# Optimization experiments

Measured on AMD Instinct MI355X. Metric: run time of the kernel, lower is better.

Reference implementation:

```python
import jax, jax.numpy as jnp
import numpy as np

N, E, HDIM, EDIM, MSG_H, UPD_H = 50000, 640000, 128, 32, 128, 128
LN_EPS = 1e-5


def setup_inputs() -> dict:
    key = jax.random.key(0)
    ks = jax.random.split(key, 12)
    def lin(k, fan_in, fan_out):
        return jax.random.normal(k, (fan_in, fan_out), dtype=jnp.float32) / np.sqrt(fan_in)
    h = jax.random.normal(ks[0], (N, HDIM), dtype=jnp.float32)
    edge_index = jax.random.randint(ks[1], (2, E), 0, N, dtype=jnp.int32)
    edge_attr = jax.random.normal(ks[2], (E, EDIM), dtype=jnp.float32)
    return {
        "h": h,
        "edge_index": edge_index,
        "edge_attr": edge_attr,
        # edge MLP: Linear(2*hdim+edim -> msg_hidden), ReLU, Linear(msg_hidden -> hdim)
        "ew1": lin(ks[3], 2 * HDIM + EDIM, MSG_H),
        "eb1": jnp.zeros((MSG_H,), jnp.float32),
        "ew2": lin(ks[4], MSG_H, HDIM),
        "eb2": jnp.zeros((HDIM,), jnp.float32),
        # node MLP: Linear(2*hdim -> upd_hidden), ReLU, Linear(upd_hidden -> hdim)
        "nw1": lin(ks[5], 2 * HDIM, UPD_H),
        "nb1": jnp.zeros((UPD_H,), jnp.float32),
        "nw2": lin(ks[6], UPD_H, HDIM),
        "nb2": jnp.zeros((HDIM,), jnp.float32),
        # LayerNorm(hdim)
        "gamma": jnp.ones((HDIM,), jnp.float32),
        "beta": jnp.zeros((HDIM,), jnp.float32),
    }


def reference(h, edge_index, edge_attr, ew1, eb1, ew2, eb2, nw1, nb1, nw2, nb2, gamma, beta):
    src, dst = edge_index[0], edge_index[1]
    # gather + concat -> edge MLP  (eval mode: dropout inactive, edge_dropout off)
    m_in = jnp.concatenate([h[src], h[dst], edge_attr], axis=1)       # [E, 2H+EDIM]
    m = jax.nn.relu(m_in @ ew1 + eb1) @ ew2 + eb2                     # [E, H]
    # scatter-add messages into destination nodes
    agg = jax.ops.segment_sum(m, dst, num_segments=h.shape[0])        # [N, H]
    # node update MLP
    u_in = jnp.concatenate([h, agg], axis=1)                          # [N, 2H]
    h_upd = jax.nn.relu(u_in @ nw1 + nb1) @ nw2 + nb2                 # [N, H]
    # residual + LayerNorm
    x = h + h_upd
    mu = jnp.mean(x, axis=-1, keepdims=True)
    var = jnp.mean(jnp.square(x - mu), axis=-1, keepdims=True)
    return (x - mu) * jax.lax.rsqrt(var + LN_EPS) * gamma + beta
```

## Files before the change

kernel.cpp:

```cpp
#include <hip/hip_runtime.h>
#include <cstdint>

#define HD 128
#define ED 32
#define BME 32
#define BMN 128
#define PAD_N 264
#define PAD_T 136
#define EGRID 512

typedef _Float16 f16;
typedef __attribute__((ext_vector_type(2))) _Float16 f16x2;
typedef __attribute__((ext_vector_type(4))) _Float16 f16x4;
typedef __attribute__((ext_vector_type(8))) _Float16 f16x8;
typedef __attribute__((ext_vector_type(4))) float    f32x4;
typedef __attribute__((ext_vector_type(4))) unsigned int u32x4;

__device__ __forceinline__ f32x4 mfma16(f16x8 a, f16x8 b, f32x4 c) {
    return __builtin_amdgcn_mfma_f32_16x16x32_f16(a, b, c, 0, 0, 0);
}
__device__ __forceinline__ f16x8 cvt8(const float* p) {
    const float4 a0 = *(const float4*)p;
    const float4 a1 = *(const float4*)(p + 4);
    f16x8 v;
    v[0] = (f16)a0.x; v[1] = (f16)a0.y; v[2] = (f16)a0.z; v[3] = (f16)a0.w;
    v[4] = (f16)a1.x; v[5] = (f16)a1.y; v[6] = (f16)a1.z; v[7] = (f16)a1.w;
    return v;
}
__device__ __forceinline__ void barrier_lds() {
    asm volatile("s_waitcnt lgkmcnt(0)" ::: "memory");
    __builtin_amdgcn_s_barrier();
    __builtin_amdgcn_sched_barrier(0);
}

__global__ __launch_bounds__(256) void zero_f32(float4* p, long n4) {
    long i = (long)blockIdx.x * blockDim.x + threadIdx.x;
    const long stride = (long)gridDim.x * blockDim.x;
    const float4 z = make_float4(0.f, 0.f, 0.f, 0.f);
    for (; i < n4; i += stride) p[i] = z;
}
__global__ __launch_bounds__(256) void zero_i32(int* p, int n) {
    int i = blockIdx.x * blockDim.x + threadIdx.x;
    if (i < n) p[i] = 0;
}
__global__ __launch_bounds__(256)
void cvt_f16_kernel(const float* __restrict__ x, f16* __restrict__ y, long n8) {
    long i = blockIdx.x * 256 + threadIdx.x;
    const long stride = (long)gridDim.x * 256;
    for (; i < n8; i += stride) *(f16x8*)(y + i * 8) = cvt8(x + i * 8);
}
__global__ __launch_bounds__(256)
void pack_all_kernel(const float* __restrict__ ew1, const float* __restrict__ ew2,
                     const float* __restrict__ nw1, const float* __restrict__ nw2,
                     f16* __restrict__ w1p, f16* __restrict__ w2p,
                     f16* __restrict__ n1p, f16* __restrict__ n2p)
{
    const int b = blockIdx.x;
    const float* w; f16* wp; int base;
    if (b < 18)      { w = ew1; wp = w1p; base = b; }
    else if (b < 26) { w = ew2; wp = w2p; base = b - 18; }
    else if (b < 42) { w = nw1; wp = n1p; base = b - 26; }
    else             { w = nw2; wp = n2p; base = b - 42; }
    const int idx = base * 256 + threadIdx.x;
    const int l  = idx & 63;
    const int fr = idx >> 6;
    const int wi = fr & 7, kt = fr >> 3;
    const int lii = l & 15, qq = l >> 4;
    const float* p = w + (size_t)(32 * kt + 8 * qq) * HD + 16 * wi + lii;
    f16x8 v;
#pragma unroll
    for (int e2 = 0; e2 < 8; ++e2) v[e2] = (f16)p[(size_t)e2 * HD];
    *(f16x8*)(wp + (size_t)idx * 8) = v;
}

__global__ __launch_bounds__(256)
void hist_kernel(const int* __restrict__ eidx, int* __restrict__ rank,
                 int* __restrict__ cnt, int E) {
    int e = blockIdx.x * 256 + threadIdx.x;
    if (e < E) rank[e] = atomicAdd(&cnt[eidx[E + e]], 1);
}
__global__ __launch_bounds__(1024)
void scan_kernel(const int* __restrict__ cnt, int* __restrict__ rs, int N) {
    __shared__ int wsum[16];
    __shared__ int s_carry;
    const int t = threadIdx.x, lane = t & 63, wid = t >> 6;
    if (t == 0) s_carry = 0;
    __syncthreads();
    for (int base = 0; base < N; base += 1024) {
        const int i = base + t;
        const int v = (i < N) ? cnt[i] : 0;
        int incl = v;
#pragma unroll
        for (int off = 1; off < 64; off <<= 1) {
            int u = __shfl_up(incl, off, 64);
            if (lane >= off) incl += u;
        }
        if (lane == 63) wsum[wid] = incl;
        __syncthreads();
        if (t == 0) {
            int s = 0;
#pragma unroll
            for (int w = 0; w < 16; ++w) { int x = wsum[w]; wsum[w] = s; s += x; }
        }
        __syncthreads();
        const int carry = s_carry;
        if (i < N) rs[i] = carry + wsum[wid] + incl - v;
        __syncthreads();
        if (t == 1023) s_carry = carry + wsum[15] + incl;
        __syncthreads();
    }
    if (threadIdx.x == 0) rs[N] = s_carry;
}
__global__ __launch_bounds__(256)
void pos_kernel(const int* __restrict__ eidx, const int* __restrict__ rs,
                int* __restrict__ pos, int E) {
    int e = blockIdx.x * 256 + threadIdx.x;
    if (e < E) pos[e] = rs[eidx[E + e]] + pos[e];
}
__global__ __launch_bounds__(256)
void inv_kernel(const int* __restrict__ pos, int* __restrict__ inv, int E) {
    int e = blockIdx.x * 256 + threadIdx.x;
    if (e < E) inv[pos[e]] = e;
}

template <int MODE>
__global__ __launch_bounds__(256, 2)
void edge_kernel(const f16*   __restrict__ h16,
                 const int*   __restrict__ eidx,
                 const float* __restrict__ ea,
                 const f16*   __restrict__ w1p,
                 const float* __restrict__ b1,
                 const f16*   __restrict__ w2p,
                 const float* __restrict__ b2,
                 void*        __restrict__ aggm,
                 const int*   __restrict__ inv,
                 int E, int ntiles)
{
    __shared__ __align__(16) f16 sA[BME * 320];
    __shared__ __align__(16) f16 sT[BME * 128];
    __shared__ int sIdx[2][BME];

    const int t  = threadIdx.x;
    const int l  = t & 63;
    const int wv = t >> 6;
    const int li = l & 15;
    const int q  = l >> 4;
    const int lm = l & 7;
    const int r  = t >> 3;
    const int q8 = t & 7;

    f16x8 A1[2][9], A2[2][4];
#pragma unroll
    for (int ht = 0; ht < 2; ++ht) {
#pragma unroll
        for (int kt = 0; kt < 9; ++kt)
            A1[ht][kt] = *(const f16x8*)(w1p + ((size_t)(kt * 8 + wv * 2 + ht) * 64 + l) * 8);
#pragma unroll
        for (int kt = 0; kt < 4; ++kt)
            A2[ht][kt] = *(const f16x8*)(w2p + ((size_t)(kt * 8 + wv * 2 + ht) * 64 + l) * 8);
    }

    f16x8 d[4];
    f16x8 d4;
    int   psr = 0;
    auto prefetch = [&](int tile) {
        const int slot = min(tile * BME + r, E - 1);
        int e;
        if (MODE == 0) e = slot;
        else           e = inv[slot];
        const int src = eidx[e];
        const int dst = eidx[E + e];
        if (MODE == 0) psr = dst;
        const f16* hs = h16 + (size_t)src * HD;
        const f16* hd = h16 + (size_t)dst * HD;
#pragma unroll
        for (int i = 0; i < 4; ++i) {
            const int c = (q8 + 8 * i) * 8;
            d[i] = (c < HD) ? *(const f16x8*)(hs + c)
                            : *(const f16x8*)(hd + (c - HD));
        }
        if (q8 < 4) d4 = cvt8(ea + (size_t)e * ED + q8 * 8);
    };

    int tb = blockIdx.x;
    if (tb < ntiles) prefetch(tb);
    int par = 0;

    for (; tb < ntiles; tb += gridDim.x, par ^= 1) {
        {
            f16* row = sA + r * 320;
            const int sw = r & 7;
#pragma unroll
            for (int i = 0; i < 4; ++i) {
                const int ch = q8 + 8 * i;
                *(f16x8*)(row + ((ch ^ sw) * 8)) = d[i];
            }
            if (q8 < 4)
                *(f16x8*)(row + (((q8 + 32) ^ sw) * 8)) = d4;
            if (MODE == 0 && q8 == 0) sIdx[par][r] = psr;
        }
        barrier_lds();

        const int nt = tb + (int)gridDim.x;
        if (nt < ntiles) prefetch(nt);

        f32x4 acc[2][2];
#pragma unroll
        for (int i = 0; i < 2; ++i)
#pragma unroll
            for (int j = 0; j < 2; ++j) acc[i][j] = (f32x4){0.f, 0.f, 0.f, 0.f};
#pragma unroll
        for (int kt = 0; kt < 9; ++kt) {
#pragma unroll
            for (int e = 0; e < 2; ++e) {
                const f16x8 b = *(const f16x8*)(sA + (16 * e + li) * 320
                                                + (((4 * kt + q) ^ lm) * 8));
                acc[0][e] = mfma16(A1[0][kt], b, acc[0][e]);
                acc[1][e] = mfma16(A1[1][kt], b, acc[1][e]);
            }
        }

#pragma unroll
        for (int ht = 0; ht < 2; ++ht) {
            const int hidb = 32 * wv + 16 * ht + 4 * q;
            const float4 bb = *(const float4*)(b1 + hidb);
            const int chT = hidb >> 3;
            const int off = hidb & 7;
#pragma unroll
            for (int e = 0; e < 2; ++e) {
                const f32x4 v = acc[ht][e];
                float x0 = fmaxf(v[0] + bb.x, 0.f), x1 = fmaxf(v[1] + bb.y, 0.f);
                float x2 = fmaxf(v[2] + bb.z, 0.f), x3 = fmaxf(v[3] + bb.w, 0.f);
                f16x4 o; o[0] = (f16)x0; o[1] = (f16)x1; o[2] = (f16)x2; o[3] = (f16)x3;
                *(f16x4*)(sT + (16 * e + li) * 128 + ((chT ^ lm) * 8) + off) = o;
            }
        }
        barrier_lds();

        f32x4 acc2[2][2];
#pragma unroll
        for (int i = 0; i < 2; ++i)
#pragma unroll
            for (int j = 0; j < 2; ++j) acc2[i][j] = (f32x4){0.f, 0.f, 0.f, 0.f};
#pragma unroll
        for (int kt = 0; kt < 4; ++kt) {
#pragma unroll
            for (int e = 0; e < 2; ++e) {
                const f16x8 b = *(const f16x8*)(sT + (16 * e + li) * 128
                                                + (((4 * kt + q) ^ lm) * 8));
                acc2[0][e] = mfma16(A2[0][kt], b, acc2[0][e]);
                acc2[1][e] = mfma16(A2[1][kt], b, acc2[1][e]);
            }
        }

        if (MODE == 0) {
            float* agg = (float*)aggm;
#pragma unroll
            for (int ht = 0; ht < 2; ++ht) {
                const int hidb = 32 * wv + 16 * ht + 4 * q;
                const float4 bb = *(const float4*)(b2 + hidb);
#pragma unroll
                for (int e = 0; e < 2; ++e) {
                    const int edge = 16 * e + li;
                    if (tb * BME + edge < E) {
                        float* p = agg + (size_t)sIdx[par][edge] * HD + hidb;
                        const f32x4 v = acc2[ht][e];
                        atomicAdd(p + 0, v[0] + bb.x);
                        atomicAdd(p + 1, v[1] + bb.y);
                        atomicAdd(p + 2, v[2] + bb.z);
                        atomicAdd(p + 3, v[3] + bb.w);
                    }
                }
            }
            barrier_lds();
        } else {
            barrier_lds();
#pragma unroll
            for (int ht = 0; ht < 2; ++ht) {
                const int hidb = 32 * wv + 16 * ht + 4 * q;
                const float4 bb = *(const float4*)(b2 + hidb);
                const int chT = hidb >> 3;
                const int off = hidb & 7;
#pragma unroll
                for (int e = 0; e < 2; ++e) {
                    const f32x4 v = acc2[ht][e];
                    f16x4 o;
                    o[0] = (f16)(v[0] + bb.x); o[1] = (f16)(v[1] + bb.y);
                    o[2] = (f16)(v[2] + bb.z); o[3] = (f16)(v[3] + bb.w);
                    *(f16x4*)(sT + (16 * e + li) * 128 + ((chT ^ lm) * 8) + off) = o;
                }
            }
            barrier_lds();
            f16* m = (f16*)aggm;
            const size_t mbase = (size_t)tb * BME * HD;
#pragma unroll
            for (int i = 0; i < 2; ++i) {
                const int idx  = t + i * 256;
                const int row2 = idx >> 4;
                const int c    = idx & 15;
                if (tb * BME + row2 < E) {
                    const f16x8 v = *(const f16x8*)(sT + row2 * 128
                                                    + ((c ^ (row2 & 7)) * 8));
                    __builtin_nontemporal_store(*(const u32x4*)&v,
                        (u32x4*)(m + mbase + (size_t)row2 * HD + c * 8));
                }
            }
        }
    }
}

template <int CSR>
__global__ __launch_bounds__(256, 2)
void node_kernel(const f16*   __restrict__ h16,
                 const float* __restrict__ h,
                 const f16*   __restrict__ m,
                 const int*   __restrict__ rs,
                 const float* __restrict__ aggf,
                 const f16*   __restrict__ w1p,
                 const float* __restrict__ b1,
                 const f16*   __restrict__ w2p,
                 const float* __restrict__ b2,
                 const float* __restrict__ gamma,
                 const float* __restrict__ beta,
                 float*       __restrict__ out,
                 int N)
{
    __shared__ __align__(16) f16 sA[BMN * PAD_N];
    __shared__ float sMV[2 * BMN];

    const int t  = threadIdx.x;
    const int l  = t & 63;
    const int wv = t >> 6;
    const int li = l & 15;
    const int q  = l >> 4;
    const int nbase = blockIdx.x * BMN;

    {
        const int r = t >> 1, half = t & 1;
        const int node = min(nbase + r, N - 1);
        f16* rowp = sA + r * PAD_N;
        {
            const f16* srcp = h16 + (size_t)node * HD + half * 64;
#pragma unroll
            for (int i = 0; i < 8; ++i)
                *(f16x8*)(rowp + half * 64 + i * 8) = *(const f16x8*)(srcp + i * 8);
        }
        if (CSR) {
            const int s = rs[node], en = rs[node + 1];
            float ag[64];
#pragma unroll
            for (int i = 0; i < 64; ++i) ag[i] = 0.f;
            const f16* base = m + (size_t)s * HD + half * 64;
            for (int j = 0; j < en - s; ++j) {
                const f16* rp = base + (size_t)j * HD;
#pragma unroll
                for (int i = 0; i < 8; ++i) {
                    const f16x8 v = *(const f16x8*)(rp + i * 8);
#pragma unroll
                    for (int k2 = 0; k2 < 8; ++k2) ag[i * 8 + k2] += (float)v[k2];
                }
            }
#pragma unroll
            for (int i = 0; i < 8; ++i) {
                f16x8 o;
#pragma unroll
                for (int k2 = 0; k2 < 8; ++k2) o[k2] = (f16)ag[i * 8 + k2];
                *(f16x8*)(rowp + 128 + half * 64 + i * 8) = o;
            }
        } else {
            const float* srcp = aggf + (size_t)node * HD + half * 64;
#pragma unroll
            for (int i = 0; i < 8; ++i)
                *(f16x8*)(rowp + 128 + half * 64 + i * 8) = cvt8(srcp + i * 8);
        }
    }
    __syncthreads();

    f16x8 A1[2][8];
#pragma unroll
    for (int ht = 0; ht < 2; ++ht)
#pragma unroll
        for (int kt = 0; kt < 8; ++kt)
            A1[ht][kt] = *(const f16x8*)(w1p + ((size_t)(kt * 8 + wv * 2 + ht) * 64 + l) * 8);

    f32x4 acc[2][8];
#pragma unroll
    for (int i = 0; i < 2; ++i)
#pragma unroll
        for (int j = 0; j < 8; ++j) acc[i][j] = (f32x4){0.f, 0.f, 0.f, 0.f};
#pragma unroll
    for (int kt = 0; kt < 8; ++kt) {
#pragma unroll
        for (int et = 0; et < 8; ++et) {
            const f16x8 b = *(const f16x8*)(sA + (16 * et + li) * PAD_N + 32 * kt + 8 * q);
            acc[0][et] = mfma16(A1[0][kt], b, acc[0][et]);
            acc[1][et] = mfma16(A1[1][kt], b, acc[1][et]);
        }
    }
    __syncthreads();

    f16x8 A2[2][4];
#pragma unroll
    for (int ht = 0; ht < 2; ++ht)
#pragma unroll
        for (int kt = 0; kt < 4; ++kt)
            A2[ht][kt] = *(const f16x8*)(w2p + ((size_t)(kt * 8 + wv * 2 + ht) * 64 + l) * 8);

    f16* sT = sA;
#pragma unroll
    for (int ht = 0; ht < 2; ++ht) {
        const int hidb = 32 * wv + 16 * ht + 4 * q;
        const float4 bb = *(const float4*)(b1 + hidb);
#pragma unroll
        for (int et = 0; et < 8; ++et) {
            const f32x4 v = acc[ht][et];
            float x0 = fmaxf(v[0] + bb.x, 0.f), x1 = fmaxf(v[1] + bb.y, 0.f);
            float x2 = fmaxf(v[2] + bb.z, 0.f), x3 = fmaxf(v[3] + bb.w, 0.f);
            f16x4 o; o[0] = (f16)x0; o[1] = (f16)x1; o[2] = (f16)x2; o[3] = (f16)x3;
            *(f16x4*)(sT + (16 * et + li) * PAD_T + hidb) = o;
        }
    }
    __syncthreads();

    f32x4 acc2[2][8];
#pragma unroll
    for (int i = 0; i < 2; ++i)
#pragma unroll
        for (int j = 0; j < 8; ++j) acc2[i][j] = (f32x4){0.f, 0.f, 0.f, 0.f};
#pragma unroll
    for (int kt = 0; kt < 4; ++kt) {
#pragma unroll
        for (int et = 0; et < 8; ++et) {
            const f16x8 b = *(const f16x8*)(sT + (16 * et + li) * PAD_T + 32 * kt + 8 * q);
            acc2[0][et] = mfma16(A2[0][kt], b, acc2[0][et]);
            acc2[1][et] = mfma16(A2[1][kt], b, acc2[1][et]);
        }
    }
    __syncthreads();

    float* sX = (float*)sA;
#pragma unroll
    for (int ht = 0; ht < 2; ++ht) {
        const int hidb = 32 * wv + 16 * ht + 4 * q;
        const float4 bb = *(const float4*)(b2 + hidb);
#pragma unroll
        for (int et = 0; et < 8; ++et) {
            const int node = 16 * et + li;
            const int nc   = min(nbase + node, N - 1);
            const float4 hv = *(const float4*)(h + (size_t)nc * HD + hidb);
            const f32x4 v = acc2[ht][et];
            f32x4 x;
            x[0] = v[0] + bb.x + hv.x;
            x[1] = v[1] + bb.y + hv.y;
            x[2] = v[2] + bb.z + hv.z;
            x[3] = v[3] + bb.w + hv.w;
            *(f32x4*)(sX + (size_t)node * 132 + hidb) = x;
        }
    }
    __syncthreads();

    {
        const int node  = t >> 1;
        const int half2 = t & 1;
        const float* px = sX + node * 132 + half2 * 64;
        float s = 0.f, sq = 0.f;
#pragma unroll
        for (int i = 0; i < 16; ++i) {
            const float4 v = *(const float4*)(px + i * 4);
            s  += v.x + v.y + v.z + v.w;
            sq += v.x * v.x + v.y * v.y + v.z * v.z + v.w * v.w;
        }
        s  += __shfl_xor(s, 1);
        sq += __shfl_xor(sq, 1);
        if (!half2) {
            const float mean = s * (1.f / HD);
            const float var  = sq * (1.f / HD) - mean * mean;
            sMV[node]       = mean;
            sMV[BMN + node] = rsqrtf(var + 1e-5f);
        }
    }
    __syncthreads();

#pragma unroll
    for (int i = 0; i < 16; ++i) {
        const int idx  = t + i * 256;
        const int node = idx >> 5;
        const int c4   = (idx & 31) * 4;
        if (nbase + node < N) {
            const float4 xv = *(const float4*)(sX + node * 132 + c4);
            const float4 g4 = *(const float4*)(gamma + c4);
            const float4 b4 = *(const float4*)(beta + c4);
            const float mean = sMV[node];
            const float rstd = sMV[BMN + node];
            float4 o;
            o.x = (xv.x - mean) * rstd * g4.x + b4.x;
            o.y = (xv.y - mean) * rstd * g4.y + b4.y;
            o.z = (xv.z - mean) * rstd * g4.z + b4.z;
            o.w = (xv.w - mean) * rstd * g4.w + b4.w;
            *(float4*)(out + (size_t)(nbase + node) * HD + c4) = o;
        }
    }
}

extern "C" void kernel_launch(void* const* d_in, const int* in_sizes, int n_in,
                              void* d_out, int out_size, void* d_ws, size_t ws_size,
                              hipStream_t stream)
{
    const float* h     = (const float*)d_in[0];
    const int*   eidx  = (const int*)  d_in[1];
    const float* ea    = (const float*)d_in[2];
    const float* ew1   = (const float*)d_in[3];
    const float* eb1   = (const float*)d_in[4];
    const float* ew2   = (const float*)d_in[5];
    const float* eb2   = (const float*)d_in[6];
    const float* nw1   = (const float*)d_in[7];
    const float* nb1   = (const float*)d_in[8];
    const float* nw2   = (const float*)d_in[9];
    const float* nb2   = (const float*)d_in[10];
    const float* gamma = (const float*)d_in[11];
    const float* beta  = (const float*)d_in[12];
    float* out = (float*)d_out;

    const int N = in_sizes[0] / HD;
    const int E = in_sizes[1] / 2;
    const int ntiles = (E + BME - 1) / BME;

    size_t off = 0;
    auto alloc = [&](size_t bytes) {
        size_t o = off; off += (bytes + 255) & ~(size_t)255; return o;
    };
    const size_t o_m    = alloc((size_t)E * HD * sizeof(f16));
    const size_t o_h16  = alloc((size_t)N * HD * sizeof(f16));
    const size_t o_pos  = alloc((size_t)E * sizeof(int));
    const size_t o_inv  = alloc((size_t)E * sizeof(int));
    const size_t o_rs   = alloc((size_t)(N + 1) * sizeof(int));
    const size_t o_cnt  = alloc((size_t)N * sizeof(int));
    const size_t o_w1p  = alloc((size_t)9 * 8 * 64 * 8 * sizeof(f16));
    const size_t o_w2p  = alloc((size_t)4 * 8 * 64 * 8 * sizeof(f16));
    const size_t o_n1p  = alloc((size_t)8 * 8 * 64 * 8 * sizeof(f16));
    const size_t o_n2p  = alloc((size_t)4 * 8 * 64 * 8 * sizeof(f16));
    const bool csr = (off <= ws_size);
    char* ws = (char*)d_ws;

    if (csr) {
        f16* mb   = (f16*)(ws + o_m);
        f16* h16  = (f16*)(ws + o_h16);
        int* pos  = (int*)(ws + o_pos);
        int* inv  = (int*)(ws + o_inv);
        int* rs   = (int*)(ws + o_rs);
        int* cnt  = (int*)(ws + o_cnt);
        f16* w1p  = (f16*)(ws + o_w1p);
        f16* w2p  = (f16*)(ws + o_w2p);
        f16* n1p  = (f16*)(ws + o_n1p);
        f16* n2p  = (f16*)(ws + o_n2p);

        zero_i32<<<(N + 255) / 256, 256, 0, stream>>>(cnt, N);
        hist_kernel<<<(E + 255) / 256, 256, 0, stream>>>(eidx, pos, cnt, E);
        scan_kernel<<<1, 1024, 0, stream>>>(cnt, rs, N);
        pos_kernel<<<(E + 255) / 256, 256, 0, stream>>>(eidx, rs, pos, E);
        inv_kernel<<<(E + 255) / 256, 256, 0, stream>>>(pos, inv, E);
        cvt_f16_kernel<<<2048, 256, 0, stream>>>(h, h16, (long)N * HD / 8);
        pack_all_kernel<<<50, 256, 0, stream>>>(ew1, ew2, nw1, nw2, w1p, w2p, n1p, n2p);
        edge_kernel<1><<<EGRID, 256, 0, stream>>>(
            h16, eidx, ea, w1p, eb1, w2p, eb2, (void*)mb, inv, E, ntiles);
        node_kernel<1><<<(N + BMN - 1) / BMN, 256, 0, stream>>>(
            h16, h, mb, rs, nullptr, n1p, nb1, n2p, nb2, gamma, beta, out, N);
    } else {
        size_t foff = 0;
        auto falloc = [&](size_t bytes) {
            size_t o = foff; foff += (bytes + 255) & ~(size_t)255; return o;
        };
        float* agg = (float*)(ws + falloc((size_t)N * HD * sizeof(float)));
        f16*   h16 = (f16*)  (ws + falloc((size_t)N * HD * sizeof(f16)));
        f16*   w1p = (f16*)  (ws + falloc((size_t)9 * 8 * 64 * 8 * sizeof(f16)));
        f16*   w2p = (f16*)  (ws + falloc((size_t)4 * 8 * 64 * 8 * sizeof(f16)));
        f16*   n1p = (f16*)  (ws + falloc((size_t)8 * 8 * 64 * 8 * sizeof(f16)));
        f16*   n2p = (f16*)  (ws + falloc((size_t)4 * 8 * 64 * 8 * sizeof(f16)));

        zero_f32<<<1024, 256, 0, stream>>>((float4*)agg, (long)N * HD / 4);
        cvt_f16_kernel<<<2048, 256, 0, stream>>>(h, h16, (long)N * HD / 8);
        pack_all_kernel<<<50, 256, 0, stream>>>(ew1, ew2, nw1, nw2, w1p, w2p, n1p, n2p);
        edge_kernel<0><<<EGRID, 256, 0, stream>>>(
            h16, eidx, ea, w1p, eb1, w2p, eb2, (void*)agg, nullptr, E, ntiles);
        node_kernel<0><<<(N + BMN - 1) / BMN, 256, 0, stream>>>(
            h16, h, nullptr, nullptr, agg, n1p, nb1, n2p, nb2, gamma, beta, out, N);
    }
}
```

Baseline: 283.2 us.

## Parallelize CSR scan, materialize sorted edge arrays, and double-buffer edge output LDS

Replaces the single-block serial-carry prefix scan with a three-kernel block-parallel scan (block sums, offsets, per-block scan). It fuses the position and inverse-permutation kernels into one kernel that writes dst-sorted src, dst and original edge id arrays directly, so the edge kernel no longer does a dependent inv[] lookup followed by an eidx gather. A separate LDS buffer for the output transpose removes one barrier in the CSR path. The cost is extra workspace, scattered writes in the fused kernel, more LDS per block and two extra kernel launches.

```diff
diff --git a/kernel.cpp b/kernel.cpp
--- a/kernel.cpp
+++ b/kernel.cpp
@@ -79,48 +79,81 @@
     int e = blockIdx.x * 256 + threadIdx.x;
     if (e < E) rank[e] = atomicAdd(&cnt[eidx[E + e]], 1);
 }
-__global__ __launch_bounds__(1024)
-void scan_kernel(const int* __restrict__ cnt, int* __restrict__ rs, int N) {
-    __shared__ int wsum[16];
-    __shared__ int s_carry;
-    const int t = threadIdx.x, lane = t & 63, wid = t >> 6;
-    if (t == 0) s_carry = 0;
-    __syncthreads();
-    for (int base = 0; base < N; base += 1024) {
-        const int i = base + t;
-        const int v = (i < N) ? cnt[i] : 0;
-        int incl = v;
-#pragma unroll
-        for (int off = 1; off < 64; off <<= 1) {
-            int u = __shfl_up(incl, off, 64);
-            if (lane >= off) incl += u;
-        }
-        if (lane == 63) wsum[wid] = incl;
-        __syncthreads();
-        if (t == 0) {
-            int s = 0;
-#pragma unroll
-            for (int w = 0; w < 16; ++w) { int x = wsum[w]; wsum[w] = s; s += x; }
-        }
-        __syncthreads();
-        const int carry = s_carry;
-        if (i < N) rs[i] = carry + wsum[wid] + incl - v;
-        __syncthreads();
-        if (t == 1023) s_carry = carry + wsum[15] + incl;
-        __syncthreads();
-    }
-    if (threadIdx.x == 0) rs[N] = s_carry;
+__global__ __launch_bounds__(256)
+void scan1_kernel(const int* __restrict__ cnt, int* __restrict__ bsum, int N) {
+    const int b = blockIdx.x, t = threadIdx.x;
+    const int base = b * 1024 + t * 4;
+    int s = 0;
+#pragma unroll
+    for (int j = 0; j < 4; ++j) { int i = base + j; s += (i < N) ? cnt[i] : 0; }
+#pragma unroll
+    for (int off = 1; off < 64; off <<= 1) s += __shfl_xor(s, off, 64);
+    __shared__ int ws[4];
+    if ((t & 63) == 0) ws[t >> 6] = s;
+    __syncthreads();
+    if (t == 0) bsum[b] = ws[0] + ws[1] + ws[2] + ws[3];
+}
+__global__ __launch_bounds__(256)
+void scan2_kernel(const int* __restrict__ bsum, int* __restrict__ boff,
+                  int* __restrict__ rs, int nb, int N) {
+    const int t = threadIdx.x, lane = t & 63, w = t >> 6;
+    int v = (t < nb) ? bsum[t] : 0;
+    int incl = v;
+#pragma unroll
+    for (int off = 1; off < 64; off <<= 1) {
+        int u = __shfl_up(incl, off, 64);
+        if (lane >= off) incl += u;
+    }
+    __shared__ int ws[4];
+    if (lane == 63) ws[w] = incl;
+    __syncthreads();
+    int wo = 0;
+    for (int k = 0; k < w; ++k) wo += ws[k];
+    const int excl = wo + incl - v;
+    if (t < nb) boff[t] = excl;
+    if (t == nb - 1) rs[N] = excl + v;
+}
+__global__ __launch_bounds__(256)
+void scan3_kernel(const int* __restrict__ cnt, const int* __restrict__ boff,
+                  int* __restrict__ rs, int N) {
+    const int b = blockIdx.x, t = threadIdx.x;
+    const int base = b * 1024 + t * 4;
+    int v[4]; int ts = 0;
+#pragma unroll
+    for (int j = 0; j < 4; ++j) { int i = base + j; v[j] = (i < N) ? cnt[i] : 0; ts += v[j]; }
+    const int lane = t & 63, w = t >> 6;
+    int incl = ts;
+#pragma unroll
+    for (int off = 1; off < 64; off <<= 1) {
+        int u = __shfl_up(incl, off, 64);
+        if (lane >= off) incl += u;
+    }
+    __shared__ int ws[4];
+    if (lane == 63) ws[w] = incl;
+    __syncthreads();
+    int wo = 0;
+    for (int k = 0; k < w; ++k) wo += ws[k];
+    int run = boff[b] + wo + incl - ts;
+#pragma unroll
+    for (int j = 0; j < 4; ++j) {
+        int i = base + j;
+        if (i < N) rs[i] = run;
+        run += v[j];
+    }
 }
 __global__ __launch_bounds__(256)
 void pos_kernel(const int* __restrict__ eidx, const int* __restrict__ rs,
-                int* __restrict__ pos, int E) {
+                const int* __restrict__ rank,
+                int* __restrict__ esrc, int* __restrict__ edst,
+                int* __restrict__ eea, int E) {
     int e = blockIdx.x * 256 + threadIdx.x;
-    if (e < E) pos[e] = rs[eidx[E + e]] + pos[e];
-}
-__global__ __launch_bounds__(256)
-void inv_kernel(const int* __restrict__ pos, int* __restrict__ inv, int E) {
-    int e = blockIdx.x * 256 + threadIdx.x;
-    if (e < E) inv[pos[e]] = e;
+    if (e < E) {
+        const int dst = eidx[E + e];
+        const int p = rs[dst] + rank[e];
+        esrc[p] = eidx[e];
+        edst[p] = dst;
+        eea[p]  = e;
+    }
 }
 
 template <int MODE>
@@ -133,11 +166,14 @@
                  const f16*   __restrict__ w2p,
                  const float* __restrict__ b2,
                  void*        __restrict__ aggm,
-                 const int*   __restrict__ inv,
+                 const int*   __restrict__ esrc,
+                 const int*   __restrict__ edst,
+                 const int*   __restrict__ eea,
                  int E, int ntiles)
 {
-    __shared__ __align__(16) f16 sA[BME * 320];
-    __shared__ __align__(16) f16 sT[BME * 128];
+    __shared__ __align__(16) f16 sA [BME * 320];
+    __shared__ __align__(16) f16 sT [BME * 128];
+    __shared__ __align__(16) f16 sTo[BME * 128];
     __shared__ int sIdx[2][BME];
 
     const int t  = threadIdx.x;
@@ -165,12 +201,12 @@
     int   psr = 0;
     auto prefetch = [&](int tile) {
         const int slot = min(tile * BME + r, E - 1);
-        int e;
-        if (MODE == 0) e = slot;
-        else           e = inv[slot];
-        const int src = eidx[e];
-        const int dst = eidx[E + e];
-        if (MODE == 0) psr = dst;
+        int src, dst, e;
+        if (MODE == 0) {
+            e = slot; src = eidx[e]; dst = eidx[E + e]; psr = dst;
+        } else {
+            src = esrc[slot]; dst = edst[slot]; e = eea[slot];
+        }
         const f16* hs = h16 + (size_t)src * HD;
         const f16* hd = h16 + (size_t)dst * HD;
 #pragma unroll
@@ -274,7 +310,6 @@
             }
             barrier_lds();
         } else {
-            barrier_lds();
 #pragma unroll
             for (int ht = 0; ht < 2; ++ht) {
                 const int hidb = 32 * wv + 16 * ht + 4 * q;
@@ -287,7 +322,7 @@
                     f16x4 o;
                     o[0] = (f16)(v[0] + bb.x); o[1] = (f16)(v[1] + bb.y);
                     o[2] = (f16)(v[2] + bb.z); o[3] = (f16)(v[3] + bb.w);
-                    *(f16x4*)(sT + (16 * e + li) * 128 + ((chT ^ lm) * 8) + off) = o;
+                    *(f16x4*)(sTo + (16 * e + li) * 128 + ((chT ^ lm) * 8) + off) = o;
                 }
             }
             barrier_lds();
@@ -299,7 +334,7 @@
                 const int row2 = idx >> 4;
                 const int c    = idx & 15;
                 if (tb * BME + row2 < E) {
-                    const f16x8 v = *(const f16x8*)(sT + row2 * 128
+                    const f16x8 v = *(const f16x8*)(sTo + row2 * 128
                                                     + ((c ^ (row2 & 7)) * 8));
                     __builtin_nontemporal_store(*(const u32x4*)&v,
                         (u32x4*)(m + mbase + (size_t)row2 * HD + c * 8));
@@ -524,6 +559,7 @@
     const int N = in_sizes[0] / HD;
     const int E = in_sizes[1] / 2;
     const int ntiles = (E + BME - 1) / BME;
+    const int nb = (N + 1023) / 1024;
 
     size_t off = 0;
     auto alloc = [&](size_t bytes) {
@@ -531,38 +567,47 @@
     };
     const size_t o_m    = alloc((size_t)E * HD * sizeof(f16));
     const size_t o_h16  = alloc((size_t)N * HD * sizeof(f16));
-    const size_t o_pos  = alloc((size_t)E * sizeof(int));
-    const size_t o_inv  = alloc((size_t)E * sizeof(int));
+    const size_t o_rank = alloc((size_t)E * sizeof(int));
+    const size_t o_es   = alloc((size_t)E * sizeof(int));
+    const size_t o_ed   = alloc((size_t)E * sizeof(int));
+    const size_t o_ee   = alloc((size_t)E * sizeof(int));
     const size_t o_rs   = alloc((size_t)(N + 1) * sizeof(int));
     const size_t o_cnt  = alloc((size_t)N * sizeof(int));
+    const size_t o_bs   = alloc((size_t)(nb + 1) * sizeof(int));
+    const size_t o_bo   = alloc((size_t)(nb + 1) * sizeof(int));
     const size_t o_w1p  = alloc((size_t)9 * 8 * 64 * 8 * sizeof(f16));
     const size_t o_w2p  = alloc((size_t)4 * 8 * 64 * 8 * sizeof(f16));
     const size_t o_n1p  = alloc((size_t)8 * 8 * 64 * 8 * sizeof(f16));
     const size_t o_n2p  = alloc((size_t)4 * 8 * 64 * 8 * sizeof(f16));
-    const bool csr = (off <= ws_size);
+    const bool csr = (off <= ws_size) && (nb <= 256);
     char* ws = (char*)d_ws;
 
     if (csr) {
         f16* mb   = (f16*)(ws + o_m);
         f16* h16  = (f16*)(ws + o_h16);
-        int* pos  = (int*)(ws + o_pos);
-        int* inv  = (int*)(ws + o_inv);
+        int* rank = (int*)(ws + o_rank);
+        int* esrc = (int*)(ws + o_es);
+        int* edst = (int*)(ws + o_ed);
+        int* eea  = (int*)(ws + o_ee);
         int* rs   = (int*)(ws + o_rs);
         int* cnt  = (int*)(ws + o_cnt);
+        int* bsum = (int*)(ws + o_bs);
+        int* boff = (int*)(ws + o_bo);
         f16* w1p  = (f16*)(ws + o_w1p);
         f16* w2p  = (f16*)(ws + o_w2p);
         f16* n1p  = (f16*)(ws + o_n1p);
         f16* n2p  = (f16*)(ws + o_n2p);
 
         zero_i32<<<(N + 255) / 256, 256, 0, stream>>>(cnt, N);
-        hist_kernel<<<(E + 255) / 256, 256, 0, stream>>>(eidx, pos, cnt, E);
-        scan_kernel<<<1, 1024, 0, stream>>>(cnt, rs, N);
-        pos_kernel<<<(E + 255) / 256, 256, 0, stream>>>(eidx, rs, pos, E);
-        inv_kernel<<<(E + 255) / 256, 256, 0, stream>>>(pos, inv, E);
+        hist_kernel<<<(E + 255) / 256, 256, 0, stream>>>(eidx, rank, cnt, E);
+        scan1_kernel<<<nb, 256, 0, stream>>>(cnt, bsum, N);
+        scan2_kernel<<<1, 256, 0, stream>>>(bsum, boff, rs, nb, N);
+        scan3_kernel<<<nb, 256, 0, stream>>>(cnt, boff, rs, N);
+        pos_kernel<<<(E + 255) / 256, 256, 0, stream>>>(eidx, rs, rank, esrc, edst, eea, E);
         cvt_f16_kernel<<<2048, 256, 0, stream>>>(h, h16, (long)N * HD / 8);
         pack_all_kernel<<<50, 256, 0, stream>>>(ew1, ew2, nw1, nw2, w1p, w2p, n1p, n2p);
         edge_kernel<1><<<EGRID, 256, 0, stream>>>(
-            h16, eidx, ea, w1p, eb1, w2p, eb2, (void*)mb, inv, E, ntiles);
+            h16, eidx, ea, w1p, eb1, w2p, eb2, (void*)mb, esrc, edst, eea, E, ntiles);
         node_kernel<1><<<(N + BMN - 1) / BMN, 256, 0, stream>>>(
             h16, h, mb, rs, nullptr, n1p, nb1, n2p, nb2, gamma, beta, out, N);
     } else {
@@ -581,7 +626,8 @@
         cvt_f16_kernel<<<2048, 256, 0, stream>>>(h, h16, (long)N * HD / 8);
         pack_all_kernel<<<50, 256, 0, stream>>>(ew1, ew2, nw1, nw2, w1p, w2p, n1p, n2p);
         edge_kernel<0><<<EGRID, 256, 0, stream>>>(
-            h16, eidx, ea, w1p, eb1, w2p, eb2, (void*)agg, nullptr, E, ntiles);
+            h16, eidx, ea, w1p, eb1, w2p, eb2, (void*)agg,
+            nullptr, nullptr, nullptr, E, ntiles);
         node_kernel<0><<<(N + BMN - 1) / BMN, 256, 0, stream>>>(
             h16, h, nullptr, nullptr, agg, n1p, nb1, n2p, nb2, gamma, beta, out, N);
     }
```

Result: faster. 268.6 us (-5.1%).
